# Kernel optimization log

Hardware: AMD Instinct MI355X
Metric: run time of the kernel (lower is better)

## Reference

```python
import jax, jax.numpy as jnp
import numpy as np

B, M, H, E, V, U = 1024, 15, 256, 256, 30000, 1000


def setup_inputs() -> dict:
    key = jax.random.key(0)
    ks = jax.random.split(key, 24)
    s = 0.05  # weight init scale
    return {
        "input_ids": jax.random.randint(ks[0], (B, 1), 0, V),
        "input_embedding": jax.random.normal(ks[1], (B, 1, E), jnp.float32),
        "hidden": jax.random.normal(ks[2], (1, B, H), jnp.float32),
        "inter_output": jax.random.normal(ks[3], (B, M, H), jnp.float32),
        "user_list": jax.random.randint(ks[4], (B,), 0, U),
        # per-user parameter tables (torch ModuleLists of Linear); stored [in,out]
        "inter_W": jax.random.normal(ks[5], (U, H, H), jnp.float32) * s,
        "inter_b": jax.random.normal(ks[6], (U, H), jnp.float32) * s,
        "hidden_W": jax.random.normal(ks[7], (U, H, H), jnp.float32) * s,
        "hidden_b": jax.random.normal(ks[8], (U, H), jnp.float32) * s,
        "lt1_W": jax.random.normal(ks[9], (U, 2 * H, H), jnp.float32) * s,
        "lt1_b": jax.random.normal(ks[10], (U, H), jnp.float32) * s,
        "scale_W": jax.random.normal(ks[11], (U, H), jnp.float32) * s,
        "scale_b": jax.random.normal(ks[12], (U,), jnp.float32) * s,
        # GRU (1 layer), torch layout: W_ih [3H, 2E], W_hh [3H, H], gate order r,z,n
        "gru_Wih": jax.random.normal(ks[13], (3 * H, 2 * E), jnp.float32) * s,
        "gru_Whh": jax.random.normal(ks[14], (3 * H, H), jnp.float32) * s,
        "gru_bih": jax.random.normal(ks[15], (3 * H,), jnp.float32) * s,
        "gru_bhh": jax.random.normal(ks[16], (3 * H,), jnp.float32) * s,
        # output projection, stored [H, V]
        "lin_W": jax.random.normal(ks[17], (H, V), jnp.float32) * s,
        "lin_b": jax.random.normal(ks[18], (V,), jnp.float32) * s,
    }


def reference(input_ids, input_embedding, hidden, inter_output, user_list,
              inter_W, inter_b, hidden_W, hidden_b, lt1_W, lt1_b,
              scale_W, scale_b, gru_Wih, gru_Whh, gru_bih, gru_bhh,
              lin_W, lin_b):
    embedded_input = input_embedding  # dropout p=0 (eval)
    hidden_t = jnp.transpose(hidden, (1, 0, 2))  # [B,1,H]

    # per-user intra attention: gather user weights, batched GEMMs (replaces python loop)
    Wi = inter_W[user_list]                      # [B,H,H]
    inter_output_a = jnp.einsum('bmh,bho->bmo', inter_output, Wi) + inter_b[user_list][:, None, :]
    Wh = hidden_W[user_list]                     # [B,H,H]
    hidden_t_a = jnp.einsum('bih,bho->bio', hidden_t, Wh) + hidden_b[user_list][:, None, :]  # [B,1,H]
    cat = jnp.concatenate([jnp.broadcast_to(hidden_t_a, (hidden_t_a.shape[0], M, H)), inter_output_a], axis=2)  # [B,M,2H]
    result = jnp.tanh(jnp.einsum('bmk,bko->bmo', cat, lt1_W[user_list]) + lt1_b[user_list][:, None, :])  # [B,M,H]
    energies = jnp.einsum('bmh,bh->bm', result, scale_W[user_list]) + scale_b[user_list][:, None]  # [B,M]

    attn_weights = jax.nn.softmax(energies, axis=1)                      # [B,M]
    context = jnp.einsum('bm,bmh->bh', attn_weights, inter_output)[:, None, :]  # [B,1,H]

    gru_input = jnp.concatenate([embedded_input, context], axis=2)  # [B,1,2E]
    x = gru_input[:, 0, :]
    h = hidden[0]
    gi = x @ gru_Wih.T + gru_bih   # [B,3H]
    gh = h @ gru_Whh.T + gru_bhh
    gi_r, gi_z, gi_n = jnp.split(gi, 3, axis=1)
    gh_r, gh_z, gh_n = jnp.split(gh, 3, axis=1)
    r = jax.nn.sigmoid(gi_r + gh_r)
    z = jax.nn.sigmoid(gi_z + gh_z)
    n = jnp.tanh(gi_n + r * gh_n)
    h_new = (1.0 - z) * n + z * h
    gru_output = h_new[:, None, :]       # [B,1,H]
    hidden_new = h_new[None, :, :]       # [1,B,H]

    output = gru_output @ lin_W + lin_b  # [B,1,V]
    return (output, hidden_new, embedded_input, gru_output, attn_weights)
```

## Files before the change

### kernel.cpp

```cpp
#include <hip/hip_runtime.h>
#include <math.h>

#define B 1024
#define M 15
#define H 256
#define E 256
#define V 30000
#define U 1000

typedef float  vf4    __attribute__((ext_vector_type(4)));
typedef __bf16 bf16x8 __attribute__((ext_vector_type(8)));
typedef float  f32x4  __attribute__((ext_vector_type(4)));

#define O_OUT   0
#define O_HID   ((size_t)B*V)
#define O_EMB   (O_HID + (size_t)B*H)
#define O_GRU   (O_EMB + (size_t)B*E)
#define O_ATT   (O_GRU + (size_t)B*H)

#define GLDS(g, l) __builtin_amdgcn_global_load_lds( \
    (const __attribute__((address_space(1))) void*)(g), \
    (__attribute__((address_space(3))) void*)(l), 16, 0, 0)

union BF8 { __bf16 h[8]; bf16x8 v; };
union BF4 { __bf16 h[4]; unsigned long long u; };

__global__ __launch_bounds__(1024) void sort_kernel(
    const int* __restrict__ ul, int* __restrict__ order)
{
    __shared__ int cnt[1024];
    __shared__ int base[1024];
    const int tid = threadIdx.x;
    cnt[tid] = 0;
    __syncthreads();
    const int u = ul[tid];
    atomicAdd(&cnt[u], 1);
    __syncthreads();
    int c0 = cnt[tid];
    int v  = c0;
    for (int off = 1; off < 1024; off <<= 1) {
        int add = (tid >= off) ? cnt[tid - off] : 0;
        __syncthreads();
        v += add;
        cnt[tid] = v;
        __syncthreads();
    }
    base[tid] = v - c0;
    __syncthreads();
    int pos = atomicAdd(&base[u], 1);
    order[pos] = tid;
}

__global__ __launch_bounds__(256, 3) void attn_kernel(
    const float* __restrict__ hidden,
    const float* __restrict__ inter_output,
    const int*   __restrict__ user_list,
    const int*   __restrict__ order,
    const float* __restrict__ inter_W,
    const float* __restrict__ inter_b,
    const float* __restrict__ hidden_W,
    const float* __restrict__ hidden_b,
    const float* __restrict__ lt1_W,
    const float* __restrict__ lt1_b,
    const float* __restrict__ scale_W,
    const float* __restrict__ scale_b,
    float* __restrict__ out,
    __bf16* __restrict__ xcat)
{
    const int s    = ((blockIdx.x & 7) << 7) + (blockIdx.x >> 3);
    const int b    = order[s];
    const int tid  = threadIdx.x;
    const int lane = tid & 63;
    const int wave = tid >> 6;
    const int wn0  = wave * 64;
    const int u    = user_list[b];

    __shared__ __align__(16) __bf16 Wt[256 * 64];
    __shared__ __align__(16) __bf16 Abuf[16 * 512];
    __shared__ float hta[H];
    __shared__ float red[64];
    __shared__ float e_lds[M];

    bf16x8 afrag[16];
    {
        const int m  = lane & 15;
        const int ko = (lane >> 4) * 8;
        #pragma unroll
        for (int t = 0; t < 16; ++t) {
            int k = t * 32 + ko;
            BF8 p;
            #pragma unroll
            for (int j = 0; j < 8; ++j) p.h[j] = (__bf16)0.f;
            if (m < 15 && k < 256) {
                vf4 f0 = *(const vf4*)&inter_output[(size_t)b * M * H + m * H + k];
                vf4 f1 = *(const vf4*)&inter_output[(size_t)b * M * H + m * H + k + 4];
                p.h[0]=(__bf16)f0[0]; p.h[1]=(__bf16)f0[1]; p.h[2]=(__bf16)f0[2]; p.h[3]=(__bf16)f0[3];
                p.h[4]=(__bf16)f1[0]; p.h[5]=(__bf16)f1[1]; p.h[6]=(__bf16)f1[2]; p.h[7]=(__bf16)f1[3];
            } else if (m == 15 && k >= 256) {
                vf4 f0 = *(const vf4*)&hidden[(size_t)b * H + (k - 256)];
                vf4 f1 = *(const vf4*)&hidden[(size_t)b * H + (k - 256) + 4];
                p.h[0]=(__bf16)f0[0]; p.h[1]=(__bf16)f0[1]; p.h[2]=(__bf16)f0[2]; p.h[3]=(__bf16)f0[3];
                p.h[4]=(__bf16)f1[0]; p.h[5]=(__bf16)f1[1]; p.h[6]=(__bf16)f1[2]; p.h[7]=(__bf16)f1[3];
            }
            afrag[t] = p.v;
        }
    }

    f32x4 acc1[4];
    #pragma unroll
    for (int nf = 0; nf < 4; ++nf) { f32x4 z = {0.f,0.f,0.f,0.f}; acc1[nf] = z; }

    const float* Wi_base  = inter_W  + (size_t)u * H * H;
    const float* Wh_base  = hidden_W + (size_t)u * H * H;
    const float* lt1_base = lt1_W    + (size_t)u * 2 * H * H;

    const int so0  = (tid & 127) * 2;
    const int shh  = (tid >> 7) * 32;
    const int skey = (so0 >> 1) & 7;

    for (int ks = 0; ks < 8; ++ks) {
        const float* Bsrc = (ks < 4) ? (Wi_base + (size_t)ks * 64 * H)
                                     : (Wh_base + (size_t)(ks - 4) * 64 * H);
        #pragma unroll
        for (int i = 0; i < 4; ++i) {
            int cl = (shh >> 3) + i;
            float2 f[8];
            #pragma unroll
            for (int j = 0; j < 8; ++j)
                f[j] = *(const float2*)&Bsrc[(size_t)(shh + i * 8 + j) * H + so0];
            BF8 p0, p1;
            #pragma unroll
            for (int j = 0; j < 8; ++j) { p0.h[j] = (__bf16)f[j].x; p1.h[j] = (__bf16)f[j].y; }
            int sc = (cl ^ skey) * 8;
            *(bf16x8*)&Wt[so0 * 64 + sc]       = p0.v;
            *(bf16x8*)&Wt[(so0 + 1) * 64 + sc] = p1.v;
        }
        __syncthreads();
        #pragma unroll
        for (int kk = 0; kk < 2; ++kk) {
            bf16x8 a = afrag[ks * 2 + kk];
            #pragma unroll
            for (int nf = 0; nf < 4; ++nf) {
                int col = wn0 + nf * 16 + (lane & 15);
                int cb  = kk * 4 + (lane >> 4);
                bf16x8 bb = *(const bf16x8*)&Wt[col * 64 + ((cb ^ ((col >> 1) & 7))) * 8];
                acc1[nf] = __builtin_amdgcn_mfma_f32_16x16x32_bf16(a, bb, acc1[nf], 0, 0, 0);
            }
        }
        __syncthreads();
    }

    if ((lane >> 4) == 3) {
        #pragma unroll
        for (int nf = 0; nf < 4; ++nf) {
            int o = wn0 + nf * 16 + (lane & 15);
            hta[o] = acc1[nf][3] + hidden_b[(size_t)u * H + o];
        }
    }
    __syncthreads();

    {
        const int m  = tid >> 4;
        const int l4 = (tid & 15) * 4;
        #pragma unroll
        for (int it = 0; it < 4; ++it) {
            int k = l4 + it * 64;
            vf4 fv = *(const vf4*)&hta[k];
            BF4 p;
            p.h[0] = (__bf16)fv[0]; p.h[1] = (__bf16)fv[1];
            p.h[2] = (__bf16)fv[2]; p.h[3] = (__bf16)fv[3];
            int sc = (k >> 3) ^ (m & 7);
            *(unsigned long long*)&Abuf[m * 512 + sc * 8 + (k & 7)] = p.u;
        }
    }
    #pragma unroll
    for (int nf = 0; nf < 4; ++nf) {
        int o  = wn0 + nf * 16 + (lane & 15);
        float bi = inter_b[(size_t)u * H + o];
        int k  = 256 + o;
        #pragma unroll
        for (int j = 0; j < 4; ++j) {
            int m  = (lane >> 4) * 4 + j;
            int sc = (k >> 3) ^ (m & 7);
            Abuf[m * 512 + sc * 8 + (k & 7)] = (__bf16)(acc1[nf][j] + bi);
        }
    }

    f32x4 acc2[4];
    #pragma unroll
    for (int nf = 0; nf < 4; ++nf) { f32x4 z = {0.f,0.f,0.f,0.f}; acc2[nf] = z; }

    for (int ks = 0; ks < 8; ++ks) {
        const float* Bsrc = lt1_base + (size_t)ks * 64 * H;
        #pragma unroll
        for (int i = 0; i < 4; ++i) {
            int cl = (shh >> 3) + i;
            float2 f[8];
            #pragma unroll
            for (int j = 0; j < 8; ++j)
                f[j] = *(const float2*)&Bsrc[(size_t)(shh + i * 8 + j) * H + so0];
            BF8 p0, p1;
            #pragma unroll
            for (int j = 0; j < 8; ++j) { p0.h[j] = (__bf16)f[j].x; p1.h[j] = (__bf16)f[j].y; }
            int sc = (cl ^ skey) * 8;
            *(bf16x8*)&Wt[so0 * 64 + sc]       = p0.v;
            *(bf16x8*)&Wt[(so0 + 1) * 64 + sc] = p1.v;
        }
        __syncthreads();
        #pragma unroll
        for (int kk = 0; kk < 2; ++kk) {
            int ca = ks * 8 + kk * 4 + (lane >> 4);
            bf16x8 a = *(const bf16x8*)&Abuf[(lane & 15) * 512 + ((ca ^ (lane & 7))) * 8];
            #pragma unroll
            for (int nf = 0; nf < 4; ++nf) {
                int col = wn0 + nf * 16 + (lane & 15);
                int cb  = kk * 4 + (lane >> 4);
                bf16x8 bb = *(const bf16x8*)&Wt[col * 64 + ((cb ^ ((col >> 1) & 7))) * 8];
                acc2[nf] = __builtin_amdgcn_mfma_f32_16x16x32_bf16(a, bb, acc2[nf], 0, 0, 0);
            }
        }
        __syncthreads();
    }

    float p[4] = {0.f, 0.f, 0.f, 0.f};
    #pragma unroll
    for (int nf = 0; nf < 4; ++nf) {
        int o = wn0 + nf * 16 + (lane & 15);
        float l1b = lt1_b[(size_t)u * H + o];
        float sw  = scale_W[(size_t)u * H + o];
        #pragma unroll
        for (int j = 0; j < 4; ++j)
            p[j] += tanhf(acc2[nf][j] + l1b) * sw;
    }
    #pragma unroll
    for (int j = 0; j < 4; ++j) {
        float v = p[j];
        v += __shfl_xor(v, 1, 64);
        v += __shfl_xor(v, 2, 64);
        v += __shfl_xor(v, 4, 64);
        v += __shfl_xor(v, 8, 64);
        if ((lane & 15) == 0) red[wave * 16 + (lane >> 4) * 4 + j] = v;
    }
    __syncthreads();
    if (tid < M)
        e_lds[tid] = red[tid] + red[16 + tid] + red[32 + tid] + red[48 + tid]
                   + scale_b[u];
    __syncthreads();

    float mx = -1e30f;
    #pragma unroll
    for (int m = 0; m < M; ++m) mx = fmaxf(mx, e_lds[m]);
    float sum = 0.f;
    float aw[M];
    #pragma unroll
    for (int m = 0; m < M; ++m) { aw[m] = expf(e_lds[m] - mx); sum += aw[m]; }
    float inv = 1.f / sum;
    if (tid < M) out[O_ATT + (size_t)b * M + tid] = aw[tid] * inv;

    float ctx = 0.f;
    #pragma unroll
    for (int m = 0; m < M; ++m)
        ctx += aw[m] * inter_output[(size_t)b * M * H + m * H + tid];
    xcat[(size_t)b * 768 + 256 + tid] = (__bf16)(ctx * inv);
}

__global__ __launch_bounds__(256) void cvt_xh_kernel(
    const float* __restrict__ emb, const float* __restrict__ hidden,
    __bf16* __restrict__ xcat, float* __restrict__ out)
{
    const int b = blockIdx.x, tid = threadIdx.x;
    float ev = emb[(size_t)b * E + tid];
    float hv = hidden[(size_t)b * H + tid];
    xcat[(size_t)b * 768 + tid]       = (__bf16)ev;
    xcat[(size_t)b * 768 + 512 + tid] = (__bf16)hv;
    out[O_EMB + (size_t)b * E + tid]  = ev;
}

__global__ __launch_bounds__(192) void wcat_kernel(
    const float* __restrict__ Wih, const float* __restrict__ Whh,
    __bf16* __restrict__ wcat)
{
    const int n = blockIdx.x;
    const int k = threadIdx.x * 4;
    vf4 v = {0.f, 0.f, 0.f, 0.f};
    if (n < 512) {
        v = (k < 512) ? *(const vf4*)&Wih[(size_t)n * 512 + k]
                      : *(const vf4*)&Whh[(size_t)n * 256 + (k - 512)];
    } else if (n < 768) {
        if (k < 512) v = *(const vf4*)&Wih[(size_t)n * 512 + k];
    } else {
        if (k >= 512) v = *(const vf4*)&Whh[(size_t)(n - 256) * 256 + (k - 512)];
    }
    BF4 p;
    p.h[0]=(__bf16)v[0]; p.h[1]=(__bf16)v[1]; p.h[2]=(__bf16)v[2]; p.h[3]=(__bf16)v[3];
    *(unsigned long long*)&wcat[(size_t)n * 768 + k] = p.u;
}

__global__ __launch_bounds__(256) void xgemm_kernel(
    const __bf16* __restrict__ xcat, const __bf16* __restrict__ wcat,
    float* __restrict__ gates)
{
    const int n0   = blockIdx.x * 256;
    const int m0   = blockIdx.y * 64;
    const int tid  = threadIdx.x;
    const int wave = tid >> 6, lane = tid & 63;
    const int wn0  = wave * 64;

    __shared__ __align__(16) __bf16 Al[64 * 64];
    __shared__ __align__(16) __bf16 Bl[256 * 64];

    f32x4 acc[4][4];
    #pragma unroll
    for (int mf = 0; mf < 4; ++mf)
        #pragma unroll
        for (int nf = 0; nf < 4; ++nf) { f32x4 z = {0.f,0.f,0.f,0.f}; acc[mf][nf] = z; }

    for (int ks = 0; ks < 12; ++ks) {
        #pragma unroll
        for (int r = 0; r < 2; ++r) {
            int L = r * 256 + tid;
            int m = L >> 3, c = L & 7;
            int sc = c ^ (m & 7);
            GLDS(xcat + (size_t)(m0 + m) * 768 + ks * 64 + sc * 8, &Al[(size_t)L * 8]);
        }
        #pragma unroll
        for (int r = 0; r < 8; ++r) {
            int L = r * 256 + tid;
            int n = L >> 3, c = L & 7;
            int sc = c ^ (n & 7);
            GLDS(wcat + (size_t)(n0 + n) * 768 + ks * 64 + sc * 8, &Bl[(size_t)L * 8]);
        }
        __syncthreads();
        #pragma unroll
        for (int kk = 0; kk < 2; ++kk) {
            bf16x8 af[4];
            #pragma unroll
            for (int mf = 0; mf < 4; ++mf) {
                int row = mf * 16 + (lane & 15);
                int c   = kk * 4 + (lane >> 4);
                af[mf] = *(const bf16x8*)&Al[row * 64 + (c ^ (row & 7)) * 8];
            }
            bf16x8 bfr[4];
            #pragma unroll
            for (int nf = 0; nf < 4; ++nf) {
                int col = wn0 + nf * 16 + (lane & 15);
                int c   = kk * 4 + (lane >> 4);
                bfr[nf] = *(const bf16x8*)&Bl[col * 64 + (c ^ (col & 7)) * 8];
            }
            #pragma unroll
            for (int mf = 0; mf < 4; ++mf)
                #pragma unroll
                for (int nf = 0; nf < 4; ++nf)
                    acc[mf][nf] = __builtin_amdgcn_mfma_f32_16x16x32_bf16(
                        af[mf], bfr[nf], acc[mf][nf], 0, 0, 0);
        }
        __syncthreads();
    }

    #pragma unroll
    for (int nf = 0; nf < 4; ++nf) {
        int n = n0 + wn0 + nf * 16 + (lane & 15);
        #pragma unroll
        for (int mf = 0; mf < 4; ++mf) {
            int rbase = m0 + mf * 16 + (lane >> 4) * 4;
            f32x4 a = acc[mf][nf];
            #pragma unroll
            for (int j = 0; j < 4; ++j)
                gates[(size_t)(rbase + j) * 1024 + n] = a[j];
        }
    }
}

__global__ __launch_bounds__(256) void gate_kernel(
    const float* __restrict__ gates,
    const float* __restrict__ hidden,
    const float* __restrict__ bih, const float* __restrict__ bhh,
    float* __restrict__ out, __bf16* __restrict__ hnb)
{
    const int b = blockIdx.x, j = threadIdx.x;
    const float* g = gates + (size_t)b * 1024;
    float rs  = g[j]       + bih[j]       + bhh[j];
    float zs  = g[256 + j] + bih[256 + j] + bhh[256 + j];
    float gin = g[512 + j] + bih[512 + j];
    float ghn = g[768 + j] + bhh[512 + j];
    float h   = hidden[(size_t)b * H + j];
    float r_  = 1.f / (1.f + expf(-rs));
    float z_  = 1.f / (1.f + expf(-zs));
    float n_  = tanhf(gin + r_ * ghn);
    float hn  = (1.f - z_) * n_ + z_ * h;
    out[O_HID + (size_t)b * H + j] = hn;
    out[O_GRU + (size_t)b * H + j] = hn;
    hnb[(size_t)b * H + j] = (__bf16)hn;
}

__global__ __launch_bounds__(256) void transpose_kernel(
    const float* __restrict__ lin_W, __bf16* __restrict__ WT)
{
    const int v0  = blockIdx.x * 240;
    const int k0  = blockIdx.y * 64;
    const int tid = threadIdx.x;
    const int lane = tid & 63, kq = tid >> 6;

    __shared__ __bf16 T[240 * 68];

    if (lane < 60) {
        #pragma unroll
        for (int i = 0; i < 4; ++i) {
            int kr = kq * 16 + i * 4;
            vf4 f0 = *(const vf4*)&lin_W[(size_t)(k0 + kr + 0) * V + v0 + lane * 4];
            vf4 f1 = *(const vf4*)&lin_W[(size_t)(k0 + kr + 1) * V + v0 + lane * 4];
            vf4 f2 = *(const vf4*)&lin_W[(size_t)(k0 + kr + 2) * V + v0 + lane * 4];
            vf4 f3 = *(const vf4*)&lin_W[(size_t)(k0 + kr + 3) * V + v0 + lane * 4];
            #pragma unroll
            for (int j = 0; j < 4; ++j) {
                BF4 pk;
                pk.h[0] = (__bf16)f0[j];
                pk.h[1] = (__bf16)f1[j];
                pk.h[2] = (__bf16)f2[j];
                pk.h[3] = (__bf16)f3[j];
                int v = lane * 4 + j;
                *(unsigned long long*)&T[v * 68 + kr] = pk.u;
            }
        }
    }
    __syncthreads();

    for (int r = 0; r < 15; ++r) {
        int L = r * 256 + tid;
        int v = L >> 4, c = L & 15;
        *(unsigned long long*)&WT[(size_t)(v0 + v) * H + k0 + c * 4] =
            *(const unsigned long long*)&T[v * 68 + c * 4];
    }
}

#define GBM 64
#define GBN 256
#define GBK 64
#define NTM 16
#define NWG ((117 + 1) * NTM)
__global__ __launch_bounds__(256) void out_mfma_kernel(
    const __bf16* __restrict__ hnb,
    const __bf16* __restrict__ WT,
    const float* __restrict__ lin_b,
    float* __restrict__ out)
{
    const int L  = blockIdx.x;
    const int s  = (L & 7) * (NWG / 8) + (L >> 3);
    const int nt = s >> 4, mt = s & 15;
    const int n0 = nt * GBN;
    const int m0 = mt * GBM;
    const int tid  = threadIdx.x;
    const int wave = tid >> 6, lane = tid & 63;

    __shared__ __bf16 Al[GBM * H];
    __shared__ __bf16 Bl[GBN * GBK];

    #pragma unroll
    for (int r = 0; r < 8; ++r) {
        int Li = r * 256 + tid;
        int m = Li >> 5;
        int c = Li & 31;
        int sc = c ^ (m & 7);
        GLDS(hnb + (size_t)(m0 + m) * H + sc * 8, &Al[(size_t)Li * 8]);
    }

    f32x4 acc[4][4];
    #pragma unroll
    for (int mf = 0; mf < 4; ++mf)
        #pragma unroll
        for (int nf = 0; nf < 4; ++nf) {
            f32x4 z = {0.f, 0.f, 0.f, 0.f};
            acc[mf][nf] = z;
        }

    const int wn0 = wave * 64;

    for (int ks = 0; ks < 4; ++ks) {
        #pragma unroll
        for (int r = 0; r < 8; ++r) {
            int Li = r * 256 + tid;
            int n = Li >> 3;
            int c = Li & 7;
            int sc = c ^ (n & 7);
            int nn = n0 + n; if (nn >= V) nn = V - 1;
            GLDS(WT + (size_t)nn * H + ks * GBK + sc * 8, &Bl[(size_t)Li * 8]);
        }
        __syncthreads();

        #pragma unroll
        for (int kk = 0; kk < 2; ++kk) {
            bf16x8 af[4];
            #pragma unroll
            for (int mf = 0; mf < 4; ++mf) {
                int row = mf * 16 + (lane & 15);
                int c   = ks * 8 + kk * 4 + (lane >> 4);
                int cs  = c ^ (row & 7);
                af[mf] = *(const bf16x8*)&Al[row * H + cs * 8];
            }
            bf16x8 bfr[4];
            #pragma unroll
            for (int nf = 0; nf < 4; ++nf) {
                int col = wn0 + nf * 16 + (lane & 15);
                int c   = kk * 4 + (lane >> 4);
                int cs  = c ^ (col & 7);
                bfr[nf] = *(const bf16x8*)&Bl[col * GBK + cs * 8];
            }
            #pragma unroll
            for (int mf = 0; mf < 4; ++mf)
                #pragma unroll
                for (int nf = 0; nf < 4; ++nf)
                    acc[mf][nf] = __builtin_amdgcn_mfma_f32_16x16x32_bf16(
                        af[mf], bfr[nf], acc[mf][nf], 0, 0, 0);
        }
        __syncthreads();
    }

    #pragma unroll
    for (int nf = 0; nf < 4; ++nf) {
        int v = n0 + wn0 + nf * 16 + (lane & 15);
        if (v < V) {
            float lb = lin_b[v];
            #pragma unroll
            for (int mf = 0; mf < 4; ++mf) {
                int rbase = m0 + mf * 16 + (lane >> 4) * 4;
                f32x4 a = acc[mf][nf];
                #pragma unroll
                for (int j = 0; j < 4; ++j)
                    out[(size_t)(rbase + j) * V + v] = a[j] + lb;
            }
        }
    }
}

extern "C" void kernel_launch(void* const* d_in, const int* in_sizes, int n_in,
                              void* d_out, int out_size, void* d_ws, size_t ws_size,
                              hipStream_t stream) {
    const float* emb    = (const float*)d_in[1];
    const float* hidden = (const float*)d_in[2];
    const float* io     = (const float*)d_in[3];
    const int*   ul     = (const int*)  d_in[4];
    const float* iW     = (const float*)d_in[5];
    const float* ib     = (const float*)d_in[6];
    const float* hW     = (const float*)d_in[7];
    const float* hb     = (const float*)d_in[8];
    const float* l1W    = (const float*)d_in[9];
    const float* l1b    = (const float*)d_in[10];
    const float* sW     = (const float*)d_in[11];
    const float* sb     = (const float*)d_in[12];
    const float* Wih    = (const float*)d_in[13];
    const float* Whh    = (const float*)d_in[14];
    const float* bih    = (const float*)d_in[15];
    const float* bhh    = (const float*)d_in[16];
    const float* lW     = (const float*)d_in[17];
    const float* lb     = (const float*)d_in[18];

    float* out = (float*)d_out;
    char* ws = (char*)d_ws;
    int*    order = (int*)ws;
    __bf16* xcat  = (__bf16*)(ws + 4096);
    __bf16* wcat  = (__bf16*)(ws + 4096 + 1572864);
    float*  gates = (float*) (ws + 4096 + 2 * 1572864);
    __bf16* hnb   = (__bf16*)(ws + 4096 + 2 * 1572864 + 4194304);
    __bf16* WT    = (__bf16*)(ws + 4096 + 2 * 1572864 + 4194304 + 524288);

    sort_kernel<<<1, 1024, 0, stream>>>(ul, order);
    attn_kernel<<<B, 256, 0, stream>>>(hidden, io, ul, order, iW, ib, hW, hb,
                                       l1W, l1b, sW, sb, out, xcat);
    cvt_xh_kernel<<<B, 256, 0, stream>>>(emb, hidden, xcat, out);
    wcat_kernel<<<1024, 192, 0, stream>>>(Wih, Whh, wcat);
    xgemm_kernel<<<dim3(4, 16), 256, 0, stream>>>(xcat, wcat, gates);
    gate_kernel<<<B, 256, 0, stream>>>(gates, hidden, bih, bhh, out, hnb);
    transpose_kernel<<<dim3(125, 4), 256, 0, stream>>>(lW, WT);
    out_mfma_kernel<<<NWG, 256, 0, stream>>>(hnb, WT, lb, out);
}
```

Before: 263.8 us.

## Pair same-user batch rows per block and load weights directly into MFMA fragments

The attention kernel now uses the user-sorted order to pair two consecutive batch rows that share a user, so each per-user weight fetch feeds MFMAs for both rows. B fragments are loaded straight from global memory into registers instead of being staged through LDS with barriers. Odd-position blocks in each user group exit early, and launch bounds rise to 4 blocks per SM. With random users across 1000 ids, few pairs share a user, so most blocks still process a single row. The register-direct loads are strided and less coalesced than the previous LDS staging.

```diff
diff --git a/kernel.cpp b/kernel.cpp
--- a/kernel.cpp
+++ b/kernel.cpp
@@ -26,7 +26,7 @@
 union BF4 { __bf16 h[4]; unsigned long long u; };
 
 __global__ __launch_bounds__(1024) void sort_kernel(
-    const int* __restrict__ ul, int* __restrict__ order)
+    const int* __restrict__ ul, int* __restrict__ order, int* __restrict__ rbase_g)
 {
     __shared__ int cnt[1024];
     __shared__ int base[1024];
@@ -45,17 +45,19 @@
         cnt[tid] = v;
         __syncthreads();
     }
-    base[tid] = v - c0;
+    base[tid]   = v - c0;
+    rbase_g[tid] = v - c0;
     __syncthreads();
     int pos = atomicAdd(&base[u], 1);
     order[pos] = tid;
 }
 
-__global__ __launch_bounds__(256, 3) void attn_kernel(
+__global__ __launch_bounds__(256, 4) void attn_kernel(
     const float* __restrict__ hidden,
     const float* __restrict__ inter_output,
     const int*   __restrict__ user_list,
     const int*   __restrict__ order,
+    const int*   __restrict__ rbase,
     const float* __restrict__ inter_W,
     const float* __restrict__ inter_b,
     const float* __restrict__ hidden_W,
@@ -67,162 +69,181 @@
     float* __restrict__ out,
     __bf16* __restrict__ xcat)
 {
-    const int s    = ((blockIdx.x & 7) << 7) + (blockIdx.x >> 3);
-    const int b    = order[s];
+    const int s   = ((blockIdx.x & 7) << 7) + (blockIdx.x >> 3);
+    const int b0  = order[s];
+    const int u   = user_list[b0];
+    if ((s - rbase[u]) & 1) return;
+    bool paired = false;
+    int  b1 = b0;
+    if (s + 1 < B) {
+        int ob = order[s + 1];
+        if (user_list[ob] == u) { paired = true; b1 = ob; }
+    }
+
     const int tid  = threadIdx.x;
     const int lane = tid & 63;
     const int wave = tid >> 6;
     const int wn0  = wave * 64;
-    const int u    = user_list[b];
-
-    __shared__ __align__(16) __bf16 Wt[256 * 64];
-    __shared__ __align__(16) __bf16 Abuf[16 * 512];
-    __shared__ float hta[H];
-    __shared__ float red[64];
-    __shared__ float e_lds[M];
-
-    bf16x8 afrag[16];
+
+    __shared__ __align__(16) __bf16 Abuf[32 * 512];
+    __shared__ __align__(16) __bf16 hta[2][256];
+    __shared__ float red[2][64];
+    __shared__ float e_lds[2][16];
+
     {
-        const int m  = lane & 15;
-        const int ko = (lane >> 4) * 8;
-        #pragma unroll
-        for (int t = 0; t < 16; ++t) {
-            int k = t * 32 + ko;
+        const int r    = tid >> 3;
+        const int part = tid & 7;
+        const int sm   = r >> 4;
+        const int mr   = r & 15;
+        const int bs   = sm ? b1 : b0;
+        const bool zr  = (sm == 1) && !paired;
+        #pragma unroll
+        for (int it = 0; it < 8; ++it) {
+            int c = part + it * 8;
+            int k = c * 8;
             BF8 p;
             #pragma unroll
             for (int j = 0; j < 8; ++j) p.h[j] = (__bf16)0.f;
-            if (m < 15 && k < 256) {
-                vf4 f0 = *(const vf4*)&inter_output[(size_t)b * M * H + m * H + k];
-                vf4 f1 = *(const vf4*)&inter_output[(size_t)b * M * H + m * H + k + 4];
-                p.h[0]=(__bf16)f0[0]; p.h[1]=(__bf16)f0[1]; p.h[2]=(__bf16)f0[2]; p.h[3]=(__bf16)f0[3];
-                p.h[4]=(__bf16)f1[0]; p.h[5]=(__bf16)f1[1]; p.h[6]=(__bf16)f1[2]; p.h[7]=(__bf16)f1[3];
-            } else if (m == 15 && k >= 256) {
-                vf4 f0 = *(const vf4*)&hidden[(size_t)b * H + (k - 256)];
-                vf4 f1 = *(const vf4*)&hidden[(size_t)b * H + (k - 256) + 4];
-                p.h[0]=(__bf16)f0[0]; p.h[1]=(__bf16)f0[1]; p.h[2]=(__bf16)f0[2]; p.h[3]=(__bf16)f0[3];
-                p.h[4]=(__bf16)f1[0]; p.h[5]=(__bf16)f1[1]; p.h[6]=(__bf16)f1[2]; p.h[7]=(__bf16)f1[3];
-            }
-            afrag[t] = p.v;
-        }
-    }
-
-    f32x4 acc1[4];
-    #pragma unroll
-    for (int nf = 0; nf < 4; ++nf) { f32x4 z = {0.f,0.f,0.f,0.f}; acc1[nf] = z; }
+            if (!zr) {
+                if (mr < 15 && k < 256) {
+                    vf4 f0 = *(const vf4*)&inter_output[(size_t)bs * M * H + mr * H + k];
+                    vf4 f1 = *(const vf4*)&inter_output[(size_t)bs * M * H + mr * H + k + 4];
+                    p.h[0]=(__bf16)f0[0]; p.h[1]=(__bf16)f0[1]; p.h[2]=(__bf16)f0[2]; p.h[3]=(__bf16)f0[3];
+                    p.h[4]=(__bf16)f1[0]; p.h[5]=(__bf16)f1[1]; p.h[6]=(__bf16)f1[2]; p.h[7]=(__bf16)f1[3];
+                } else if (mr == 15 && k >= 256) {
+                    vf4 f0 = *(const vf4*)&hidden[(size_t)bs * H + (k - 256)];
+                    vf4 f1 = *(const vf4*)&hidden[(size_t)bs * H + (k - 256) + 4];
+                    p.h[0]=(__bf16)f0[0]; p.h[1]=(__bf16)f0[1]; p.h[2]=(__bf16)f0[2]; p.h[3]=(__bf16)f0[3];
+                    p.h[4]=(__bf16)f1[0]; p.h[5]=(__bf16)f1[1]; p.h[6]=(__bf16)f1[2]; p.h[7]=(__bf16)f1[3];
+                }
+            }
+            *(bf16x8*)&Abuf[r * 512 + (c ^ (r & 7)) * 8] = p.v;
+        }
+    }
+    __syncthreads();
 
     const float* Wi_base  = inter_W  + (size_t)u * H * H;
     const float* Wh_base  = hidden_W + (size_t)u * H * H;
     const float* lt1_base = lt1_W    + (size_t)u * 2 * H * H;
 
-    const int so0  = (tid & 127) * 2;
-    const int shh  = (tid >> 7) * 32;
-    const int skey = (so0 >> 1) & 7;
-
-    for (int ks = 0; ks < 8; ++ks) {
-        const float* Bsrc = (ks < 4) ? (Wi_base + (size_t)ks * 64 * H)
-                                     : (Wh_base + (size_t)(ks - 4) * 64 * H);
-        #pragma unroll
-        for (int i = 0; i < 4; ++i) {
-            int cl = (shh >> 3) + i;
-            float2 f[8];
-            #pragma unroll
-            for (int j = 0; j < 8; ++j)
-                f[j] = *(const float2*)&Bsrc[(size_t)(shh + i * 8 + j) * H + so0];
-            BF8 p0, p1;
-            #pragma unroll
-            for (int j = 0; j < 8; ++j) { p0.h[j] = (__bf16)f[j].x; p1.h[j] = (__bf16)f[j].y; }
-            int sc = (cl ^ skey) * 8;
-            *(bf16x8*)&Wt[so0 * 64 + sc]       = p0.v;
-            *(bf16x8*)&Wt[(so0 + 1) * 64 + sc] = p1.v;
-        }
-        __syncthreads();
-        #pragma unroll
-        for (int kk = 0; kk < 2; ++kk) {
-            bf16x8 a = afrag[ks * 2 + kk];
-            #pragma unroll
-            for (int nf = 0; nf < 4; ++nf) {
-                int col = wn0 + nf * 16 + (lane & 15);
-                int cb  = kk * 4 + (lane >> 4);
-                bf16x8 bb = *(const bf16x8*)&Wt[col * 64 + ((cb ^ ((col >> 1) & 7))) * 8];
-                acc1[nf] = __builtin_amdgcn_mfma_f32_16x16x32_bf16(a, bb, acc1[nf], 0, 0, 0);
-            }
-        }
-        __syncthreads();
-    }
+    const int ocol = wn0 + (lane & 15);
+    const int krow = (lane >> 4) * 8;
+
+    f32x4 acc1[2][4];
+    #pragma unroll
+    for (int mf = 0; mf < 2; ++mf)
+        #pragma unroll
+        for (int nf = 0; nf < 4; ++nf) { f32x4 z = {0.f,0.f,0.f,0.f}; acc1[mf][nf] = z; }
+
+    #pragma unroll 2
+    for (int ks = 0; ks < 16; ++ks) {
+        const float* Bp = ((ks < 8) ? (Wi_base + (size_t)(ks * 32) * H)
+                                    : (Wh_base + (size_t)((ks - 8) * 32) * H))
+                          + (size_t)krow * H + ocol;
+        float t[4][8];
+        #pragma unroll
+        for (int j = 0; j < 8; ++j)
+            #pragma unroll
+            for (int nf = 0; nf < 4; ++nf)
+                t[nf][j] = Bp[(size_t)j * H + nf * 16];
+        bf16x8 bfr[4];
+        #pragma unroll
+        for (int nf = 0; nf < 4; ++nf) {
+            BF8 pk;
+            #pragma unroll
+            for (int j = 0; j < 8; ++j) pk.h[j] = (__bf16)t[nf][j];
+            bfr[nf] = pk.v;
+        }
+        int sca = ((ks * 4 + (lane >> 4)) ^ (lane & 7)) * 8;
+        bf16x8 a0 = *(const bf16x8*)&Abuf[(lane & 15) * 512 + sca];
+        #pragma unroll
+        for (int nf = 0; nf < 4; ++nf)
+            acc1[0][nf] = __builtin_amdgcn_mfma_f32_16x16x32_bf16(a0, bfr[nf], acc1[0][nf], 0, 0, 0);
+        if (paired) {
+            bf16x8 a1 = *(const bf16x8*)&Abuf[(16 + (lane & 15)) * 512 + sca];
+            #pragma unroll
+            for (int nf = 0; nf < 4; ++nf)
+                acc1[1][nf] = __builtin_amdgcn_mfma_f32_16x16x32_bf16(a1, bfr[nf], acc1[1][nf], 0, 0, 0);
+        }
+    }
+    __syncthreads();
 
     if ((lane >> 4) == 3) {
         #pragma unroll
         for (int nf = 0; nf < 4; ++nf) {
             int o = wn0 + nf * 16 + (lane & 15);
-            hta[o] = acc1[nf][3] + hidden_b[(size_t)u * H + o];
+            float hb = hidden_b[(size_t)u * H + o];
+            hta[0][o] = (__bf16)(acc1[0][nf][3] + hb);
+            hta[1][o] = (__bf16)(acc1[1][nf][3] + hb);
+        }
+    }
+    #pragma unroll
+    for (int mf = 0; mf < 2; ++mf) {
+        #pragma unroll
+        for (int nf = 0; nf < 4; ++nf) {
+            int o  = wn0 + nf * 16 + (lane & 15);
+            float bi = inter_b[(size_t)u * H + o];
+            int k  = 256 + o;
+            #pragma unroll
+            for (int j = 0; j < 4; ++j) {
+                int r  = mf * 16 + (lane >> 4) * 4 + j;
+                Abuf[r * 512 + ((k >> 3) ^ (r & 7)) * 8 + (k & 7)] = (__bf16)(acc1[mf][nf][j] + bi);
+            }
         }
     }
     __syncthreads();
 
     {
-        const int m  = tid >> 4;
-        const int l4 = (tid & 15) * 4;
+        const int r    = tid >> 3;
+        const int part = tid & 7;
+        const int sm   = r >> 4;
         #pragma unroll
         for (int it = 0; it < 4; ++it) {
-            int k = l4 + it * 64;
-            vf4 fv = *(const vf4*)&hta[k];
-            BF4 p;
-            p.h[0] = (__bf16)fv[0]; p.h[1] = (__bf16)fv[1];
-            p.h[2] = (__bf16)fv[2]; p.h[3] = (__bf16)fv[3];
-            int sc = (k >> 3) ^ (m & 7);
-            *(unsigned long long*)&Abuf[m * 512 + sc * 8 + (k & 7)] = p.u;
-        }
-    }
-    #pragma unroll
-    for (int nf = 0; nf < 4; ++nf) {
-        int o  = wn0 + nf * 16 + (lane & 15);
-        float bi = inter_b[(size_t)u * H + o];
-        int k  = 256 + o;
-        #pragma unroll
-        for (int j = 0; j < 4; ++j) {
-            int m  = (lane >> 4) * 4 + j;
-            int sc = (k >> 3) ^ (m & 7);
-            Abuf[m * 512 + sc * 8 + (k & 7)] = (__bf16)(acc1[nf][j] + bi);
-        }
-    }
-
-    f32x4 acc2[4];
-    #pragma unroll
-    for (int nf = 0; nf < 4; ++nf) { f32x4 z = {0.f,0.f,0.f,0.f}; acc2[nf] = z; }
-
-    for (int ks = 0; ks < 8; ++ks) {
-        const float* Bsrc = lt1_base + (size_t)ks * 64 * H;
-        #pragma unroll
-        for (int i = 0; i < 4; ++i) {
-            int cl = (shh >> 3) + i;
-            float2 f[8];
-            #pragma unroll
-            for (int j = 0; j < 8; ++j)
-                f[j] = *(const float2*)&Bsrc[(size_t)(shh + i * 8 + j) * H + so0];
-            BF8 p0, p1;
-            #pragma unroll
-            for (int j = 0; j < 8; ++j) { p0.h[j] = (__bf16)f[j].x; p1.h[j] = (__bf16)f[j].y; }
-            int sc = (cl ^ skey) * 8;
-            *(bf16x8*)&Wt[so0 * 64 + sc]       = p0.v;
-            *(bf16x8*)&Wt[(so0 + 1) * 64 + sc] = p1.v;
-        }
-        __syncthreads();
-        #pragma unroll
-        for (int kk = 0; kk < 2; ++kk) {
-            int ca = ks * 8 + kk * 4 + (lane >> 4);
-            bf16x8 a = *(const bf16x8*)&Abuf[(lane & 15) * 512 + ((ca ^ (lane & 7))) * 8];
-            #pragma unroll
-            for (int nf = 0; nf < 4; ++nf) {
-                int col = wn0 + nf * 16 + (lane & 15);
-                int cb  = kk * 4 + (lane >> 4);
-                bf16x8 bb = *(const bf16x8*)&Wt[col * 64 + ((cb ^ ((col >> 1) & 7))) * 8];
-                acc2[nf] = __builtin_amdgcn_mfma_f32_16x16x32_bf16(a, bb, acc2[nf], 0, 0, 0);
-            }
-        }
-        __syncthreads();
-    }
-
-    float p[4] = {0.f, 0.f, 0.f, 0.f};
+            int c = part + it * 8;
+            bf16x8 hv = *(const bf16x8*)&hta[sm][c * 8];
+            *(bf16x8*)&Abuf[r * 512 + (c ^ (r & 7)) * 8] = hv;
+        }
+    }
+    __syncthreads();
+
+    f32x4 acc2[2][4];
+    #pragma unroll
+    for (int mf = 0; mf < 2; ++mf)
+        #pragma unroll
+        for (int nf = 0; nf < 4; ++nf) { f32x4 z = {0.f,0.f,0.f,0.f}; acc2[mf][nf] = z; }
+
+    #pragma unroll 2
+    for (int ks = 0; ks < 16; ++ks) {
+        const float* Bp = lt1_base + (size_t)(ks * 32) * H + (size_t)krow * H + ocol;
+        float t[4][8];
+        #pragma unroll
+        for (int j = 0; j < 8; ++j)
+            #pragma unroll
+            for (int nf = 0; nf < 4; ++nf)
+                t[nf][j] = Bp[(size_t)j * H + nf * 16];
+        bf16x8 bfr[4];
+        #pragma unroll
+        for (int nf = 0; nf < 4; ++nf) {
+            BF8 pk;
+            #pragma unroll
+            for (int j = 0; j < 8; ++j) pk.h[j] = (__bf16)t[nf][j];
+            bfr[nf] = pk.v;
+        }
+        int sca = ((ks * 4 + (lane >> 4)) ^ (lane & 7)) * 8;
+        bf16x8 a0 = *(const bf16x8*)&Abuf[(lane & 15) * 512 + sca];
+        #pragma unroll
+        for (int nf = 0; nf < 4; ++nf)
+            acc2[0][nf] = __builtin_amdgcn_mfma_f32_16x16x32_bf16(a0, bfr[nf], acc2[0][nf], 0, 0, 0);
+        if (paired) {
+            bf16x8 a1 = *(const bf16x8*)&Abuf[(16 + (lane & 15)) * 512 + sca];
+            #pragma unroll
+            for (int nf = 0; nf < 4; ++nf)
+                acc2[1][nf] = __builtin_amdgcn_mfma_f32_16x16x32_bf16(a1, bfr[nf], acc2[1][nf], 0, 0, 0);
+        }
+    }
+
+    float p0[4] = {0.f,0.f,0.f,0.f};
+    float p1[4] = {0.f,0.f,0.f,0.f};
     #pragma unroll
     for (int nf = 0; nf < 4; ++nf) {
         int o = wn0 + nf * 16 + (lane & 15);
@@ -230,38 +251,49 @@
         float sw  = scale_W[(size_t)u * H + o];
         #pragma unroll
         for (int j = 0; j < 4; ++j)
-            p[j] += tanhf(acc2[nf][j] + l1b) * sw;
+            p0[j] += tanhf(acc2[0][nf][j] + l1b) * sw;
+        if (paired)
+            #pragma unroll
+            for (int j = 0; j < 4; ++j)
+                p1[j] += tanhf(acc2[1][nf][j] + l1b) * sw;
     }
     #pragma unroll
     for (int j = 0; j < 4; ++j) {
-        float v = p[j];
-        v += __shfl_xor(v, 1, 64);
-        v += __shfl_xor(v, 2, 64);
-        v += __shfl_xor(v, 4, 64);
-        v += __shfl_xor(v, 8, 64);
-        if ((lane & 15) == 0) red[wave * 16 + (lane >> 4) * 4 + j] = v;
-    }
-    __syncthreads();
-    if (tid < M)
-        e_lds[tid] = red[tid] + red[16 + tid] + red[32 + tid] + red[48 + tid]
-                   + scale_b[u];
-    __syncthreads();
-
-    float mx = -1e30f;
-    #pragma unroll
-    for (int m = 0; m < M; ++m) mx = fmaxf(mx, e_lds[m]);
-    float sum = 0.f;
-    float aw[M];
-    #pragma unroll
-    for (int m = 0; m < M; ++m) { aw[m] = expf(e_lds[m] - mx); sum += aw[m]; }
-    float inv = 1.f / sum;
-    if (tid < M) out[O_ATT + (size_t)b * M + tid] = aw[tid] * inv;
-
-    float ctx = 0.f;
-    #pragma unroll
-    for (int m = 0; m < M; ++m)
-        ctx += aw[m] * inter_output[(size_t)b * M * H + m * H + tid];
-    xcat[(size_t)b * 768 + 256 + tid] = (__bf16)(ctx * inv);
+        float v = p0[j];
+        v += __shfl_xor(v, 1, 64); v += __shfl_xor(v, 2, 64);
+        v += __shfl_xor(v, 4, 64); v += __shfl_xor(v, 8, 64);
+        if ((lane & 15) == 0) red[0][wave * 16 + (lane >> 4) * 4 + j] = v;
+        float w = p1[j];
+        w += __shfl_xor(w, 1, 64); w += __shfl_xor(w, 2, 64);
+        w += __shfl_xor(w, 4, 64); w += __shfl_xor(w, 8, 64);
+        if ((lane & 15) == 0) red[1][wave * 16 + (lane >> 4) * 4 + j] = w;
+    }
+    __syncthreads();
+    if (tid < 32) {
+        int sm = tid >> 4, mm = tid & 15;
+        e_lds[sm][mm] = red[sm][mm] + red[sm][16 + mm] + red[sm][32 + mm] + red[sm][48 + mm]
+                      + scale_b[u];
+    }
+    __syncthreads();
+
+    const int nsm = paired ? 2 : 1;
+    for (int sm = 0; sm < nsm; ++sm) {
+        const int bs = sm ? b1 : b0;
+        float mx = -1e30f;
+        #pragma unroll
+        for (int m = 0; m < M; ++m) mx = fmaxf(mx, e_lds[sm][m]);
+        float sum = 0.f;
+        float aw[M];
+        #pragma unroll
+        for (int m = 0; m < M; ++m) { aw[m] = expf(e_lds[sm][m] - mx); sum += aw[m]; }
+        float inv = 1.f / sum;
+        if (tid < M) out[O_ATT + (size_t)bs * M + tid] = aw[tid] * inv;
+        float ctx = 0.f;
+        #pragma unroll
+        for (int m = 0; m < M; ++m)
+            ctx += aw[m] * inter_output[(size_t)bs * M * H + m * H + tid];
+        xcat[(size_t)bs * 768 + 256 + tid] = (__bf16)(ctx * inv);
+    }
 }
 
 __global__ __launch_bounds__(256) void cvt_xh_kernel(
@@ -362,11 +394,11 @@
         int n = n0 + wn0 + nf * 16 + (lane & 15);
         #pragma unroll
         for (int mf = 0; mf < 4; ++mf) {
-            int rbase = m0 + mf * 16 + (lane >> 4) * 4;
+            int rbase_ = m0 + mf * 16 + (lane >> 4) * 4;
             f32x4 a = acc[mf][nf];
             #pragma unroll
             for (int j = 0; j < 4; ++j)
-                gates[(size_t)(rbase + j) * 1024 + n] = a[j];
+                gates[(size_t)(rbase_ + j) * 1024 + n] = a[j];
         }
     }
 }
@@ -522,11 +554,11 @@
             float lb = lin_b[v];
             #pragma unroll
             for (int mf = 0; mf < 4; ++mf) {
-                int rbase = m0 + mf * 16 + (lane >> 4) * 4;
+                int rbase_ = m0 + mf * 16 + (lane >> 4) * 4;
                 f32x4 a = acc[mf][nf];
                 #pragma unroll
                 for (int j = 0; j < 4; ++j)
-                    out[(size_t)(rbase + j) * V + v] = a[j] + lb;
+                    out[(size_t)(rbase_ + j) * V + v] = a[j] + lb;
             }
         }
     }
@@ -557,14 +589,15 @@
     float* out = (float*)d_out;
     char* ws = (char*)d_ws;
     int*    order = (int*)ws;
-    __bf16* xcat  = (__bf16*)(ws + 4096);
-    __bf16* wcat  = (__bf16*)(ws + 4096 + 1572864);
-    float*  gates = (float*) (ws + 4096 + 2 * 1572864);
-    __bf16* hnb   = (__bf16*)(ws + 4096 + 2 * 1572864 + 4194304);
-    __bf16* WT    = (__bf16*)(ws + 4096 + 2 * 1572864 + 4194304 + 524288);
-
-    sort_kernel<<<1, 1024, 0, stream>>>(ul, order);
-    attn_kernel<<<B, 256, 0, stream>>>(hidden, io, ul, order, iW, ib, hW, hb,
+    int*    rbase = (int*)(ws + 4096);
+    __bf16* xcat  = (__bf16*)(ws + 8192);
+    __bf16* wcat  = (__bf16*)(ws + 8192 + 1572864);
+    float*  gates = (float*) (ws + 8192 + 2 * 1572864);
+    __bf16* hnb   = (__bf16*)(ws + 8192 + 2 * 1572864 + 4194304);
+    __bf16* WT    = (__bf16*)(ws + 8192 + 2 * 1572864 + 4194304 + 524288);
+
+    sort_kernel<<<1, 1024, 0, stream>>>(ul, order, rbase);
+    attn_kernel<<<B, 256, 0, stream>>>(hidden, io, ul, order, rbase, iW, ib, hW, hb,
                                        l1W, l1b, sW, sb, out, xcat);
     cvt_xh_kernel<<<B, 256, 0, stream>>>(emb, hidden, xcat, out);
     wcat_kernel<<<1024, 192, 0, stream>>>(Wih, Whh, wcat);
```

Measured after the change: 253.6 us. -3.9%, faster.
